# Kernel tuning notes

Measured on AMD Instinct MI355X. Metric: run time of the kernel, lower is better.

Reference implementation:

```python
import jax, jax.numpy as jnp
import numpy as np

KH, KW, STRIDE, PAD, DIL = 3, 3, 1, 1, 1


def setup_inputs() -> dict:
    key = jax.random.key(0)
    ks = jax.random.split(key, 4)
    B, C, H, W, O = 4, 256, 64, 64, 256
    K = KH * KW
    x = jax.random.normal(ks[0], (B, C, H, W), jnp.float32)
    # offset/mask conv params (original inits to zero; use small random so offsets are non-trivial)
    w_om = jax.random.normal(ks[1], (3 * K, C, KH, KW), jnp.float32) * 0.01
    b_om = jnp.zeros((3 * K,), jnp.float32)
    # main weight: kaiming_uniform_(a=1) -> gain = sqrt(2/(1+1^2)) = 1, bound = sqrt(3)/sqrt(fan_in)
    fan_in = C * K
    bound = float(np.sqrt(3.0) / np.sqrt(fan_in))
    weight = jax.random.uniform(ks[2], (O, C, KH, KW), jnp.float32, -bound, bound)
    bias = jnp.zeros((O,), jnp.float32)
    return {"x": x, "w_om": w_om, "b_om": b_om, "weight": weight, "bias": bias}


def _deform_conv2d(x, offset, mask, weight, bias):
    # torchvision.ops.deform_conv2d semantics, deformable_groups=1, stride=1, pad=1, dil=1
    B, C, H, W = x.shape
    K = KH * KW
    # torchvision offset layout: per-tap interleaved (y, x) pairs along channel dim
    off_y = offset[:, 0::2]  # [B, K, H, W]
    off_x = offset[:, 1::2]  # [B, K, H, W]
    ky = (jnp.repeat(jnp.arange(KH), KW) * DIL).astype(x.dtype)  # [K]
    kx = (jnp.tile(jnp.arange(KW), KH) * DIL).astype(x.dtype)    # [K]
    base_y = (jnp.arange(H) * STRIDE - PAD).astype(x.dtype)
    base_x = (jnp.arange(W) * STRIDE - PAD).astype(x.dtype)
    py = base_y[None, None, :, None] + ky[None, :, None, None] + off_y  # [B,K,H,W]
    px = base_x[None, None, None, :] + kx[None, :, None, None] + off_x  # [B,K,H,W]
    y0 = jnp.floor(py)
    x0 = jnp.floor(px)
    ly = py - y0
    lx = px - x0
    y0i = y0.astype(jnp.int32)
    x0i = x0.astype(jnp.int32)
    x_flat = x.reshape(B, C, H * W)

    def gather(yy, xx):
        # zero-padded gather of one bilinear corner -> [B, C, K, H, W]
        valid = ((yy >= 0) & (yy < H) & (xx >= 0) & (xx < W)).astype(x.dtype)
        idx = (jnp.clip(yy, 0, H - 1) * W + jnp.clip(xx, 0, W - 1)).reshape(B, -1)
        g = jax.vmap(lambda xf, i: jnp.take(xf, i, axis=1))(x_flat, idx)
        return g.reshape(B, C, K, H, W) * valid.reshape(B, 1, K, H, W)

    w00 = ((1 - ly) * (1 - lx))[:, None]
    w01 = ((1 - ly) * lx)[:, None]
    w10 = (ly * (1 - lx))[:, None]
    w11 = (ly * lx)[:, None]
    val = (gather(y0i, x0i) * w00 + gather(y0i, x0i + 1) * w01
           + gather(y0i + 1, x0i) * w10 + gather(y0i + 1, x0i + 1) * w11)
    cols = val * mask[:, None]  # modulated columns [B,C,K,H,W]
    out = jnp.einsum('bckhw,ock->bohw', cols, weight.reshape(weight.shape[0], C, K))
    return out + bias[None, :, None, None]


def reference(x, w_om, b_om, weight, bias):
    om = jax.lax.conv_general_dilated(
        x, w_om, (STRIDE, STRIDE), ((PAD, PAD), (PAD, PAD)),
        rhs_dilation=(DIL, DIL), dimension_numbers=('NCHW', 'OIHW', 'NCHW'),
    ) + b_om[None, :, None, None]
    K = KH * KW
    o1, o2, m = om[:, :K], om[:, K:2 * K], om[:, 2 * K:]
    offset = jnp.concatenate([o1, o2], axis=1)  # [B, 2K, H, W]
    mask = jax.nn.sigmoid(m)                    # [B, K, H, W]
    return _deform_conv2d(x, offset, mask, weight, bias)
```

## Files before the change

### kernel.cpp

```cpp
#include <hip/hip_runtime.h>
#include <stdint.h>

#define B_ 4
#define C_ 256
#define H_ 64
#define W_ 64
#define O_ 256
#define K_ 9
#define CK 2304
#define HW 4096
#define NTOT 16384

typedef __bf16 bf16x8 __attribute__((ext_vector_type(8)));
typedef __bf16 bf16x4 __attribute__((ext_vector_type(4)));
typedef float f32x4 __attribute__((ext_vector_type(4)));
typedef float f32x2 __attribute__((ext_vector_type(2)));
typedef f32x2 __attribute__((aligned(4))) f32x2u;

__device__ __forceinline__ uint16_t f2bf(float f) {
  uint32_t u = __builtin_bit_cast(uint32_t, f);
  return (uint16_t)((u + 0x7FFFu + ((u >> 16) & 1u)) >> 16);
}

__device__ __forceinline__ uint32_t pk_bf16(float a, float b) {
  uint16_t lo = __builtin_bit_cast(uint16_t, (__bf16)a);
  uint16_t hi = __builtin_bit_cast(uint16_t, (__bf16)b);
  return (uint32_t)lo | ((uint32_t)hi << 16);
}

__global__ void k0_wconv(const float* __restrict__ weight, uint16_t* __restrict__ wb) {
  int idx = blockIdx.x * 256 + threadIdx.x;
  if (idx >= O_ * CK) return;
  int o = idx / CK;
  int rem = idx - o * CK;
  int k = rem >> 8;
  int c = rem & 255;
  wb[idx] = f2bf(weight[(o * C_ + c) * K_ + k]);
}

__global__ void k0b_womb(const float* __restrict__ w_om, uint16_t* __restrict__ womb) {
  int idx = blockIdx.x * 256 + threadIdx.x;
  if (idx >= 32 * CK) return;
  int j = idx / CK;
  int ck = idx - j * CK;
  int k = ck >> 8, c = ck & 255;
  womb[idx] = (j < 27) ? f2bf(w_om[(j * 256 + c) * 9 + k]) : (uint16_t)0;
}

__global__ void k2a_xT(const float* __restrict__ x, uint16_t* __restrict__ xT) {
  int bx = blockIdx.x;
  int ct = bx & 3;
  int hwt = (bx >> 2) & 63;
  int b = bx >> 8;
  int t = threadIdx.x;
  int l = t & 63;
  int cq = t >> 6;

  __shared__ __align__(16) uint16_t tile[64 * 72];

  const float* xb = x + ((b * 256 + ct * 64) * HW) + hwt * 64;
#pragma unroll
  for (int i = 0; i < 16; ++i) {
    int c = cq * 16 + i;
    tile[l * 72 + c] = f2bf(xb[c * HW + l]);
  }
  __syncthreads();

  int hw = t >> 2;
  int c8 = (t & 3) * 8;
  uint16_t* dst = xT + ((size_t)b << 20) + (size_t)(hwt * 64 + hw) * 256 + ct * 64;
  *(uint4*)&dst[c8] = *(const uint4*)&tile[hw * 72 + c8];
  *(uint4*)&dst[c8 + 32] = *(const uint4*)&tile[hw * 72 + c8 + 32];
}

__global__ void k1_mfma(const uint16_t* __restrict__ womb, const uint16_t* __restrict__ xT,
                        float* __restrict__ ompart) {
  int bx = blockIdx.x;
  int ks = bx >> 8;
  int nt = bx & 255;
  int t = threadIdx.x;
  int lane = t & 63;
  int wid = t >> 6;
  int lr = lane & 15, q = lane >> 4;
  int n = nt * 64 + wid * 16 + lr;
  int b = n >> 12;
  int hw = n & 4095;
  int y = hw >> 6, xx = hw & 63;
  const uint16_t* xb = xT + ((size_t)b << 20);
  const uint16_t* zrow = womb + 31 * CK;

  f32x4 acc0 = {0.f, 0.f, 0.f, 0.f};
  f32x4 acc1 = {0.f, 0.f, 0.f, 0.f};

  for (int kk = 0; kk < 3; ++kk) {
    int k = ks * 3 + kk;
    int dy = k / 3, dx = k - dy * 3;
    int ny = y + dy - 1, nx = xx + dx - 1;
    bool valid = ((unsigned)ny < 64u) && ((unsigned)nx < 64u);
    int row = (min(max(ny, 0), 63) << 6) + min(max(nx, 0), 63);
    const uint16_t* bp = valid ? (xb + row * 256 + q * 8) : (zrow + q * 8);
    const uint16_t* ap = womb + lr * CK + k * 256 + q * 8;
#pragma unroll
    for (int kt = 0; kt < 8; ++kt) {
      int c0 = kt * 32;
      bf16x8 bF = *(const bf16x8*)&bp[c0];
      bf16x8 aF0 = *(const bf16x8*)&ap[c0];
      bf16x8 aF1 = *(const bf16x8*)&ap[16 * CK + c0];
      acc0 = __builtin_amdgcn_mfma_f32_16x16x32_bf16(aF0, bF, acc0, 0, 0, 0);
      acc1 = __builtin_amdgcn_mfma_f32_16x16x32_bf16(aF1, bF, acc1, 0, 0, 0);
    }
  }

  float* op = ompart + ks * (32 * NTOT);
#pragma unroll
  for (int r = 0; r < 4; ++r) {
    op[(q * 4 + r) * NTOT + n] = acc0[r];
    op[(16 + q * 4 + r) * NTOT + n] = acc1[r];
  }
}

__global__ void k1b_ppm(const float* __restrict__ ompart, const float* __restrict__ b_om,
                        float* __restrict__ pypxmk) {
  int tid = blockIdx.x * 256 + threadIdx.x;
  int k = tid >> 14;
  int n = tid & 16383;
  int b = n >> 12;
  int hw = n & 4095;
  int h = hw >> 6, w = hw & 63;
  const float* p0 = ompart;
  const float* p1 = ompart + 32 * NTOT;
  const float* p2 = ompart + 64 * NTOT;
  int iy = (2 * k) * NTOT + n;
  int ix = (2 * k + 1) * NTOT + n;
  int im = (18 + k) * NTOT + n;
  float oy = p0[iy] + p1[iy] + p2[iy] + b_om[2 * k];
  float ox = p0[ix] + p1[ix] + p2[ix] + b_om[2 * k + 1];
  float m = p0[im] + p1[im] + p2[im] + b_om[18 + k];
  int off = (b * 9 + k) * HW + hw;
  pypxmk[off] = (float)(h - 1 + k / 3) + oy;
  pypxmk[147456 + off] = (float)(w - 1 + k % 3) + ox;
  pypxmk[294912 + off] = 1.f / (1.f + __expf(-m));
}

__global__ void k1_offconv(const float* __restrict__ x, const float* __restrict__ w_om,
                           const float* __restrict__ b_om, float* __restrict__ pypxmk) {
  int bx = blockIdx.x;
  int jq = bx % 7;
  int h = (bx / 7) % H_;
  int b = bx / (7 * H_);
  int t = threadIdx.x;
  int w = t & 63;
  int cs = __builtin_amdgcn_readfirstlane(t >> 6);

  float acc[4] = {0.f, 0.f, 0.f, 0.f};
  const float* xb = x + (b * C_) * HW;

  for (int ci = 0; ci < 64; ++ci) {
    int c = cs * 64 + ci;
    const float* xr = xb + c * HW;
    float xv[3][3];
#pragma unroll
    for (int r = 0; r < 3; ++r) {
      int y = h - 1 + r;
      bool yv = ((unsigned)y < 64u);
#pragma unroll
      for (int dx = 0; dx < 3; ++dx) {
        int xx = w - 1 + dx;
        bool v = yv && ((unsigned)xx < 64u);
        xv[r][dx] = v ? xr[y * 64 + xx] : 0.f;
      }
    }
    const float* wp = w_om + ((jq * 4) * C_ + c) * 9;
#pragma unroll
    for (int jj = 0; jj < 4; ++jj) {
      int j = jq * 4 + jj;
      int jeff = (j < 27) ? jj : 0;
      const float* wj = wp + jeff * (C_ * 9);
      float a = 0.f;
#pragma unroll
      for (int r = 0; r < 3; ++r)
#pragma unroll
        for (int dx = 0; dx < 3; ++dx)
          a = fmaf(xv[r][dx], wj[r * 3 + dx], a);
      acc[jj] += a;
    }
  }

  __shared__ float red[4][4][64];
#pragma unroll
  for (int jj = 0; jj < 4; ++jj) red[cs][jj][w] = acc[jj];
  __syncthreads();

  int jj = t >> 6;
  int j = jq * 4 + jj;
  if (j < 27) {
    float s = red[0][jj][w] + red[1][jj][w] + red[2][jj][w] + red[3][jj][w] + b_om[j];
    float* pyA = pypxmk;
    float* pxA = pypxmk + 147456;
    float* mkA = pypxmk + 294912;
    if (j < 18) {
      int k = j >> 1;
      int off = (b * 9 + k) * HW + h * 64 + w;
      if ((j & 1) == 0)
        pyA[off] = (float)(h - 1 + k / 3) + s;
      else
        pxA[off] = (float)(w - 1 + k % 3) + s;
    } else {
      int k = j - 18;
      mkA[(b * 9 + k) * HW + h * 64 + w] = 1.f / (1.f + __expf(-s));
    }
  }
}

__global__ void k2_cols(const uint16_t* __restrict__ xT, const float* __restrict__ pypxmk,
                        uint16_t* __restrict__ cols) {
  int bx = blockIdx.x;
  int g = __builtin_amdgcn_readfirstlane(threadIdx.x >> 6);
  int lane = threadIdx.x & 63;

  const float* pyA = pypxmk;
  const float* pxA = pypxmk + 147456;
  const float* mkA = pypxmk + 294912;

  for (int it = 0; it < 18; ++it) {
    int p = it * 4 + g;
    int pn = p / 9;
    int k = p - pn * 9;
    int n = (bx << 3) + pn;
    int b = n >> 12;
    int hw = n & 4095;
    int poff = (b * 9 + k) * HW + hw;
    float py = pyA[poff];
    float px = pxA[poff];
    float mk = mkA[poff];

    float fy0 = floorf(py), fx0 = floorf(px);
    float ly = py - fy0, lx = px - fx0;
    int y0 = (int)fy0, x0 = (int)fx0;
    bool vy0 = ((unsigned)y0 < 64u), vy1 = ((unsigned)(y0 + 1) < 64u);
    bool vx0 = ((unsigned)x0 < 64u), vx1 = ((unsigned)(x0 + 1) < 64u);
    float w00 = (vy0 && vx0) ? (1.f - ly) * (1.f - lx) * mk : 0.f;
    float w01 = (vy0 && vx1) ? (1.f - ly) * lx * mk : 0.f;
    float w10 = (vy1 && vx0) ? ly * (1.f - lx) * mk : 0.f;
    float w11 = (vy1 && vx1) ? ly * lx * mk : 0.f;
    bool sel0 = (x0 >= 63);
    bool sel1 = (x0 >= 0);
    float wa0 = (sel0 ? 0.f : w00) + (sel1 ? 0.f : w01);
    float wb0 = (sel0 ? w00 : 0.f) + (sel1 ? w01 : 0.f);
    float wa1 = (sel0 ? 0.f : w10) + (sel1 ? 0.f : w11);
    float wb1 = (sel0 ? w10 : 0.f) + (sel1 ? w11 : 0.f);
    int bx0 = min(max(x0, 0), 62);
    int a0 = min(max(y0, 0), 63) * 64 + bx0;
    int a1 = min(max(y0 + 1, 0), 63) * 64 + bx0;

    const uint16_t* xb = xT + ((size_t)b << 20);
    bf16x4 r00 = *(const bf16x4*)&xb[a0 * 256 + lane * 4];
    bf16x4 r01 = *(const bf16x4*)&xb[a0 * 256 + 256 + lane * 4];
    bf16x4 r10 = *(const bf16x4*)&xb[a1 * 256 + lane * 4];
    bf16x4 r11 = *(const bf16x4*)&xb[a1 * 256 + 256 + lane * 4];

    float v[4];
#pragma unroll
    for (int i = 0; i < 4; ++i)
      v[i] = wa0 * (float)r00[i] + wb0 * (float)r01[i] +
             wa1 * (float)r10[i] + wb1 * (float)r11[i];

    uint2 pk;
    pk.x = pk_bf16(v[0], v[1]);
    pk.y = pk_bf16(v[2], v[3]);
    *(uint2*)&cols[(size_t)n * CK + k * 256 + lane * 4] = pk;
  }
}

__global__ void k2_fb(const float* __restrict__ x, const float* __restrict__ pypxmk,
                      uint16_t* __restrict__ cols) {
  int bx = blockIdx.x;
  int cg = bx & 15;
  int h = (bx >> 4) & 63;
  int b = bx >> 10;
  int t = threadIdx.x;
  int w = t & 63;
  int g = t >> 6;

  const float* pyA = pypxmk;
  const float* pxA = pypxmk + 147456;
  const float* mkA = pypxmk + 294912;

  __shared__ uint16_t tile[64 * 146];
  const float* xb = x + b * C_ * HW;
  int cbase = cg * 16 + g * 4;

#pragma unroll
  for (int k = 0; k < 9; ++k) {
    int poff = (b * 9 + k) * HW + h * 64 + w;
    float py = pyA[poff];
    float px = pxA[poff];
    float mk = mkA[poff];
    float fy0 = floorf(py), fx0 = floorf(px);
    float ly = py - fy0, lx = px - fx0;
    int y0 = (int)fy0, x0 = (int)fx0;
    bool vy0 = ((unsigned)y0 < 64u), vy1 = ((unsigned)(y0 + 1) < 64u);
    bool vx0 = ((unsigned)x0 < 64u), vx1 = ((unsigned)(x0 + 1) < 64u);
    float w00 = (vy0 && vx0) ? (1.f - ly) * (1.f - lx) * mk : 0.f;
    float w01 = (vy0 && vx1) ? (1.f - ly) * lx * mk : 0.f;
    float w10 = (vy1 && vx0) ? ly * (1.f - lx) * mk : 0.f;
    float w11 = (vy1 && vx1) ? ly * lx * mk : 0.f;
    bool sel0 = (x0 >= 63);
    bool sel1 = (x0 >= 0);
    float wa0 = (sel0 ? 0.f : w00) + (sel1 ? 0.f : w01);
    float wb0 = (sel0 ? w00 : 0.f) + (sel1 ? w01 : 0.f);
    float wa1 = (sel0 ? 0.f : w10) + (sel1 ? 0.f : w11);
    float wb1 = (sel0 ? w10 : 0.f) + (sel1 ? w11 : 0.f);
    int bx0 = min(max(x0, 0), 62);
    int a0 = min(max(y0, 0), 63) * 64 + bx0;
    int a1 = min(max(y0 + 1, 0), 63) * 64 + bx0;

#pragma unroll
    for (int cp = 0; cp < 2; ++cp) {
      const float* xcA = xb + (cbase + cp * 2) * HW;
      const float* xcB = xcA + HW;
      f32x2 A0 = *(const f32x2u*)&xcA[a0];
      f32x2 A1 = *(const f32x2u*)&xcA[a1];
      f32x2 B0 = *(const f32x2u*)&xcB[a0];
      f32x2 B1 = *(const f32x2u*)&xcB[a1];
      float rA = wa0 * A0.x + wb0 * A0.y + wa1 * A1.x + wb1 * A1.y;
      float rB = wa0 * B0.x + wb0 * B0.y + wa1 * B1.x + wb1 * B1.y;
      *(uint32_t*)&tile[w * 146 + k * 16 + g * 4 + cp * 2] = pk_bf16(rA, rB);
    }
  }
  __syncthreads();

#pragma unroll
  for (int it = 0; it < 18; ++it) {
    int u = t + it * 256;
    int wu = u / 72;
    int rem = u - wu * 72;
    int k = rem >> 3;
    int cd = rem & 7;
    uint32_t val = *(const uint32_t*)&tile[wu * 146 + rem * 2];
    int n = b * HW + h * 64 + wu;
    int dst = n * CK + k * 256 + cg * 16 + cd * 2;
    *(uint32_t*)&cols[dst] = val;
  }
}

__global__ void k3_gemm(const uint16_t* __restrict__ wb, const uint16_t* __restrict__ cols,
                        const float* __restrict__ bias, float* __restrict__ dst,
                        int ktn, int withBias) {
  int bx = blockIdx.x;
  int ks = bx >> 8;
  int bxx = bx & 255;
  int mt = bxx & 1;
  int nt = bxx >> 1;
  int o0 = mt * 128;
  int n0 = nt * 128;
  int t = threadIdx.x;
  int lane = t & 63;
  int wid = t >> 6;
  int wm = wid >> 1, wn = wid & 1;
  int lr = lane & 15, q = lane >> 4;

  __shared__ __align__(16) uint16_t As[128 * 32];
  __shared__ __align__(16) uint16_t Bs[128 * 32];

  f32x4 acc[4][4];
  const f32x4 zero = {0.f, 0.f, 0.f, 0.f};
#pragma unroll
  for (int i = 0; i < 4; ++i)
#pragma unroll
    for (int j = 0; j < 4; ++j) acc[i][j] = zero;

  int r0 = t >> 2;
  int koff = (t & 3) * 8;
  int kb = ks * ktn * 32;
  const uint16_t* gA = wb + (o0 + r0) * CK + kb + koff;
  const uint16_t* gB = cols + (n0 + r0) * CK + kb + koff;

  for (int kt = 0; kt < ktn; ++kt) {
    int k0 = kt * 32;
    __builtin_amdgcn_global_load_lds(
        (const __attribute__((address_space(1))) uint32_t*)(gA + k0),
        (__attribute__((address_space(3))) uint32_t*)&As[t * 8], 16, 0, 0);
    __builtin_amdgcn_global_load_lds(
        (const __attribute__((address_space(1))) uint32_t*)(gA + 64 * CK + k0),
        (__attribute__((address_space(3))) uint32_t*)&As[2048 + t * 8], 16, 0, 0);
    __builtin_amdgcn_global_load_lds(
        (const __attribute__((address_space(1))) uint32_t*)(gB + k0),
        (__attribute__((address_space(3))) uint32_t*)&Bs[t * 8], 16, 0, 0);
    __builtin_amdgcn_global_load_lds(
        (const __attribute__((address_space(1))) uint32_t*)(gB + 64 * CK + k0),
        (__attribute__((address_space(3))) uint32_t*)&Bs[2048 + t * 8], 16, 0, 0);
    __syncthreads();

    bf16x8 aF[4], bF[4];
#pragma unroll
    for (int i = 0; i < 4; ++i)
      aF[i] = *(const bf16x8*)&As[(wm * 64 + i * 16 + lr) * 32 + q * 8];
#pragma unroll
    for (int j = 0; j < 4; ++j)
      bF[j] = *(const bf16x8*)&Bs[(wn * 64 + j * 16 + lr) * 32 + q * 8];
#pragma unroll
    for (int i = 0; i < 4; ++i)
#pragma unroll
      for (int j = 0; j < 4; ++j)
        acc[i][j] = __builtin_amdgcn_mfma_f32_16x16x32_bf16(aF[i], bF[j], acc[i][j], 0, 0, 0);
    __syncthreads();
  }

  float* base = dst + ks * (O_ * NTOT);
  int bb = n0 >> 12;
  int hw0 = n0 & 4095;
#pragma unroll
  for (int i = 0; i < 4; ++i) {
#pragma unroll
    for (int r = 0; r < 4; ++r) {
      int o = o0 + wm * 64 + i * 16 + q * 4 + r;
      float bv = withBias ? bias[o] : 0.f;
      float* orow = base + (bb * O_ + o) * HW + hw0;
#pragma unroll
      for (int j = 0; j < 4; ++j) orow[wn * 64 + j * 16 + lr] = acc[i][j][r] + bv;
    }
  }
}

__global__ void k4_reduce(const float* __restrict__ part, const float* __restrict__ bias,
                          float* __restrict__ out) {
  int i4 = blockIdx.x * 256 + threadIdx.x;
  const f32x4* p0 = (const f32x4*)part;
  const f32x4* p1 = p0 + (O_ * NTOT / 4);
  const f32x4* p2 = p1 + (O_ * NTOT / 4);
  f32x4 a = p0[i4] + p1[i4] + p2[i4];
  int o = (i4 >> 10) & 255;
  ((f32x4*)out)[i4] = a + bias[o];
}

extern "C" void kernel_launch(void* const* d_in, const int* in_sizes, int n_in,
                              void* d_out, int out_size, void* d_ws, size_t ws_size,
                              hipStream_t stream) {
  const float* x = (const float*)d_in[0];
  const float* w_om = (const float*)d_in[1];
  const float* b_om = (const float*)d_in[2];
  const float* weight = (const float*)d_in[3];
  const float* bias = (const float*)d_in[4];
  float* out = (float*)d_out;

  char* ws = (char*)d_ws;
  float* pypxmk = (float*)ws;
  uint16_t* wb = (uint16_t*)(ws + 1769472);
  uint16_t* cols = (uint16_t*)(ws + 2949120);
  uint16_t* xT = (uint16_t*)(ws + 78446592);
  uint16_t* womb = (uint16_t*)(ws + 86835200);
  float* ompart = (float*)(ws + 86982656);
  float* part = (float*)(ws + 93274112);

  bool xtpath = ws_size >= 86835200ull;
  bool mfmak1 = ws_size >= 93274112ull;
  bool splitk = ws_size >= 143605760ull;

  hipLaunchKernelGGL(k0_wconv, dim3(2304), dim3(256), 0, stream, weight, wb);

  if (xtpath) hipLaunchKernelGGL(k2a_xT, dim3(1024), dim3(256), 0, stream, x, xT);

  if (xtpath && mfmak1) {
    hipLaunchKernelGGL(k0b_womb, dim3(288), dim3(256), 0, stream, w_om, womb);
    hipLaunchKernelGGL(k1_mfma, dim3(768), dim3(256), 0, stream, womb, xT, ompart);
    hipLaunchKernelGGL(k1b_ppm, dim3(576), dim3(256), 0, stream, ompart, b_om, pypxmk);
  } else {
    hipLaunchKernelGGL(k1_offconv, dim3(4 * 64 * 7), dim3(256), 0, stream, x, w_om, b_om, pypxmk);
  }

  if (xtpath) {
    hipLaunchKernelGGL(k2_cols, dim3(2048), dim3(256), 0, stream, xT, pypxmk, cols);
  } else {
    hipLaunchKernelGGL(k2_fb, dim3(4 * 64 * 16), dim3(256), 0, stream, x, pypxmk, cols);
  }

  if (splitk) {
    hipLaunchKernelGGL(k3_gemm, dim3(768), dim3(256), 0, stream, wb, cols, bias, part, 24, 0);
    hipLaunchKernelGGL(k4_reduce, dim3(4096), dim3(256), 0, stream, part, bias, out);
  } else {
    hipLaunchKernelGGL(k3_gemm, dim3(256), dim3(256), 0, stream, wb, cols, bias, out, 72, 1);
  }
}
```

Baseline: 180.4 us.

## Fuse prep kernels, fold offset reduction into cols, drop split-K GEMM

Merges the three conversion kernels (weight, offset-weight, x transpose) into one launch. Folds the offset/mask partial-sum reduction and sigmoid into the column-sampling kernel, removing the separate ppm pass and its intermediate buffer. Replaces the split-K GEMM plus reduce with a single full-K GEMM using 128x64 tiles and 512 blocks, which avoids writing and re-reading partial outputs. The trade-off is longer per-block K loops and recomputing the three-way sum once per tap inside the cols kernel.

```diff
diff --git a/kernel.cpp b/kernel.cpp
--- a/kernel.cpp
+++ b/kernel.cpp
@@ -28,49 +28,47 @@
   return (uint32_t)lo | ((uint32_t)hi << 16);
 }
 
-__global__ void k0_wconv(const float* __restrict__ weight, uint16_t* __restrict__ wb) {
-  int idx = blockIdx.x * 256 + threadIdx.x;
-  if (idx >= O_ * CK) return;
-  int o = idx / CK;
-  int rem = idx - o * CK;
-  int k = rem >> 8;
-  int c = rem & 255;
-  wb[idx] = f2bf(weight[(o * C_ + c) * K_ + k]);
-}
-
-__global__ void k0b_womb(const float* __restrict__ w_om, uint16_t* __restrict__ womb) {
-  int idx = blockIdx.x * 256 + threadIdx.x;
-  if (idx >= 32 * CK) return;
-  int j = idx / CK;
-  int ck = idx - j * CK;
-  int k = ck >> 8, c = ck & 255;
-  womb[idx] = (j < 27) ? f2bf(w_om[(j * 256 + c) * 9 + k]) : (uint16_t)0;
-}
-
-__global__ void k2a_xT(const float* __restrict__ x, uint16_t* __restrict__ xT) {
-  int bx = blockIdx.x;
-  int ct = bx & 3;
-  int hwt = (bx >> 2) & 63;
-  int b = bx >> 8;
+__global__ void kA_prep(const float* __restrict__ weight, const float* __restrict__ w_om,
+                        const float* __restrict__ x, uint16_t* __restrict__ wb,
+                        uint16_t* __restrict__ womb, uint16_t* __restrict__ xT) {
+  int bx = blockIdx.x;
   int t = threadIdx.x;
-  int l = t & 63;
-  int cq = t >> 6;
-
-  __shared__ __align__(16) uint16_t tile[64 * 72];
-
-  const float* xb = x + ((b * 256 + ct * 64) * HW) + hwt * 64;
-#pragma unroll
-  for (int i = 0; i < 16; ++i) {
-    int c = cq * 16 + i;
-    tile[l * 72 + c] = f2bf(xb[c * HW + l]);
-  }
-  __syncthreads();
-
-  int hw = t >> 2;
-  int c8 = (t & 3) * 8;
-  uint16_t* dst = xT + ((size_t)b << 20) + (size_t)(hwt * 64 + hw) * 256 + ct * 64;
-  *(uint4*)&dst[c8] = *(const uint4*)&tile[hw * 72 + c8];
-  *(uint4*)&dst[c8 + 32] = *(const uint4*)&tile[hw * 72 + c8 + 32];
+  if (bx < 2304) {
+    int idx = bx * 256 + t;
+    int o = idx / CK;
+    int rem = idx - o * CK;
+    int k = rem >> 8, c = rem & 255;
+    wb[idx] = f2bf(weight[(o * C_ + c) * K_ + k]);
+  } else if (bx < 2592) {
+    int idx = (bx - 2304) * 256 + t;
+    int j = idx / CK;
+    int ck = idx - j * CK;
+    int k = ck >> 8, c = ck & 255;
+    womb[idx] = (j < 27) ? f2bf(w_om[(j * 256 + c) * 9 + k]) : (uint16_t)0;
+  } else {
+    int bxl = bx - 2592;
+    int ct = bxl & 3;
+    int hwt = (bxl >> 2) & 63;
+    int b = bxl >> 8;
+    int l = t & 63;
+    int cq = t >> 6;
+
+    __shared__ __align__(16) uint16_t tile[64 * 72];
+
+    const float* xb = x + ((b * 256 + ct * 64) * HW) + hwt * 64;
+#pragma unroll
+    for (int i = 0; i < 16; ++i) {
+      int c = cq * 16 + i;
+      tile[l * 72 + c] = f2bf(xb[c * HW + l]);
+    }
+    __syncthreads();
+
+    int hw = t >> 2;
+    int c8 = (t & 3) * 8;
+    uint16_t* dst = xT + ((size_t)b << 20) + (size_t)(hwt * 64 + hw) * 256 + ct * 64;
+    *(uint4*)&dst[c8] = *(const uint4*)&tile[hw * 72 + c8];
+    *(uint4*)&dst[c8 + 32] = *(const uint4*)&tile[hw * 72 + c8 + 32];
+  }
 }
 
 __global__ void k1_mfma(const uint16_t* __restrict__ womb, const uint16_t* __restrict__ xT,
@@ -119,108 +117,15 @@
   }
 }
 
-__global__ void k1b_ppm(const float* __restrict__ ompart, const float* __restrict__ b_om,
-                        float* __restrict__ pypxmk) {
-  int tid = blockIdx.x * 256 + threadIdx.x;
-  int k = tid >> 14;
-  int n = tid & 16383;
-  int b = n >> 12;
-  int hw = n & 4095;
-  int h = hw >> 6, w = hw & 63;
-  const float* p0 = ompart;
-  const float* p1 = ompart + 32 * NTOT;
-  const float* p2 = ompart + 64 * NTOT;
-  int iy = (2 * k) * NTOT + n;
-  int ix = (2 * k + 1) * NTOT + n;
-  int im = (18 + k) * NTOT + n;
-  float oy = p0[iy] + p1[iy] + p2[iy] + b_om[2 * k];
-  float ox = p0[ix] + p1[ix] + p2[ix] + b_om[2 * k + 1];
-  float m = p0[im] + p1[im] + p2[im] + b_om[18 + k];
-  int off = (b * 9 + k) * HW + hw;
-  pypxmk[off] = (float)(h - 1 + k / 3) + oy;
-  pypxmk[147456 + off] = (float)(w - 1 + k % 3) + ox;
-  pypxmk[294912 + off] = 1.f / (1.f + __expf(-m));
-}
-
-__global__ void k1_offconv(const float* __restrict__ x, const float* __restrict__ w_om,
-                           const float* __restrict__ b_om, float* __restrict__ pypxmk) {
-  int bx = blockIdx.x;
-  int jq = bx % 7;
-  int h = (bx / 7) % H_;
-  int b = bx / (7 * H_);
-  int t = threadIdx.x;
-  int w = t & 63;
-  int cs = __builtin_amdgcn_readfirstlane(t >> 6);
-
-  float acc[4] = {0.f, 0.f, 0.f, 0.f};
-  const float* xb = x + (b * C_) * HW;
-
-  for (int ci = 0; ci < 64; ++ci) {
-    int c = cs * 64 + ci;
-    const float* xr = xb + c * HW;
-    float xv[3][3];
-#pragma unroll
-    for (int r = 0; r < 3; ++r) {
-      int y = h - 1 + r;
-      bool yv = ((unsigned)y < 64u);
-#pragma unroll
-      for (int dx = 0; dx < 3; ++dx) {
-        int xx = w - 1 + dx;
-        bool v = yv && ((unsigned)xx < 64u);
-        xv[r][dx] = v ? xr[y * 64 + xx] : 0.f;
-      }
-    }
-    const float* wp = w_om + ((jq * 4) * C_ + c) * 9;
-#pragma unroll
-    for (int jj = 0; jj < 4; ++jj) {
-      int j = jq * 4 + jj;
-      int jeff = (j < 27) ? jj : 0;
-      const float* wj = wp + jeff * (C_ * 9);
-      float a = 0.f;
-#pragma unroll
-      for (int r = 0; r < 3; ++r)
-#pragma unroll
-        for (int dx = 0; dx < 3; ++dx)
-          a = fmaf(xv[r][dx], wj[r * 3 + dx], a);
-      acc[jj] += a;
-    }
-  }
-
-  __shared__ float red[4][4][64];
-#pragma unroll
-  for (int jj = 0; jj < 4; ++jj) red[cs][jj][w] = acc[jj];
-  __syncthreads();
-
-  int jj = t >> 6;
-  int j = jq * 4 + jj;
-  if (j < 27) {
-    float s = red[0][jj][w] + red[1][jj][w] + red[2][jj][w] + red[3][jj][w] + b_om[j];
-    float* pyA = pypxmk;
-    float* pxA = pypxmk + 147456;
-    float* mkA = pypxmk + 294912;
-    if (j < 18) {
-      int k = j >> 1;
-      int off = (b * 9 + k) * HW + h * 64 + w;
-      if ((j & 1) == 0)
-        pyA[off] = (float)(h - 1 + k / 3) + s;
-      else
-        pxA[off] = (float)(w - 1 + k % 3) + s;
-    } else {
-      int k = j - 18;
-      mkA[(b * 9 + k) * HW + h * 64 + w] = 1.f / (1.f + __expf(-s));
-    }
-  }
-}
-
-__global__ void k2_cols(const uint16_t* __restrict__ xT, const float* __restrict__ pypxmk,
-                        uint16_t* __restrict__ cols) {
+__global__ void k2_cols(const uint16_t* __restrict__ xT, const float* __restrict__ ompart,
+                        const float* __restrict__ b_om, uint16_t* __restrict__ cols) {
   int bx = blockIdx.x;
   int g = __builtin_amdgcn_readfirstlane(threadIdx.x >> 6);
   int lane = threadIdx.x & 63;
 
-  const float* pyA = pypxmk;
-  const float* pxA = pypxmk + 147456;
-  const float* mkA = pypxmk + 294912;
+  const float* op0 = ompart;
+  const float* op1 = ompart + 32 * NTOT;
+  const float* op2 = ompart + 64 * NTOT;
 
   for (int it = 0; it < 18; ++it) {
     int p = it * 4 + g;
@@ -229,10 +134,18 @@
     int n = (bx << 3) + pn;
     int b = n >> 12;
     int hw = n & 4095;
-    int poff = (b * 9 + k) * HW + hw;
-    float py = pyA[poff];
-    float px = pxA[poff];
-    float mk = mkA[poff];
+    int h = hw >> 6, w = hw & 63;
+
+    int iy = (2 * k) * NTOT + n;
+    int ix = iy + NTOT;
+    int im = (18 + k) * NTOT + n;
+    float oy = op0[iy] + op1[iy] + op2[iy] + b_om[2 * k];
+    float ox = op0[ix] + op1[ix] + op2[ix] + b_om[2 * k + 1];
+    float m = op0[im] + op1[im] + op2[im] + b_om[18 + k];
+    int dy = k / 3, dx = k - dy * 3;
+    float py = (float)(h - 1 + dy) + oy;
+    float px = (float)(w - 1 + dx) + ox;
+    float mk = 1.f / (1.f + __expf(-m));
 
     float fy0 = floorf(py), fx0 = floorf(px);
     float ly = py - fy0, lx = px - fx0;
@@ -269,6 +182,157 @@
     pk.x = pk_bf16(v[0], v[1]);
     pk.y = pk_bf16(v[2], v[3]);
     *(uint2*)&cols[(size_t)n * CK + k * 256 + lane * 4] = pk;
+  }
+}
+
+__global__ void k3_gemm(const uint16_t* __restrict__ wb, const uint16_t* __restrict__ cols,
+                        const float* __restrict__ bias, float* __restrict__ out) {
+  int bx = blockIdx.x;
+  int mt = bx & 1;
+  int nt = bx >> 1;
+  int o0 = mt * 128;
+  int n0 = nt * 64;
+  int t = threadIdx.x;
+  int lane = t & 63;
+  int wid = t >> 6;
+  int wm = wid >> 1, wn = wid & 1;
+  int lr = lane & 15, q = lane >> 4;
+
+  __shared__ __align__(16) uint16_t As[128 * 32];
+  __shared__ __align__(16) uint16_t Bs[64 * 32];
+
+  f32x4 acc[4][2];
+  const f32x4 zero = {0.f, 0.f, 0.f, 0.f};
+#pragma unroll
+  for (int i = 0; i < 4; ++i)
+#pragma unroll
+    for (int j = 0; j < 2; ++j) acc[i][j] = zero;
+
+  int r0 = t >> 2;
+  int koff = (t & 3) * 8;
+  const uint16_t* gA = wb + (o0 + r0) * CK + koff;
+  const uint16_t* gB = cols + (n0 + r0) * CK + koff;
+
+  for (int kt = 0; kt < 72; ++kt) {
+    int k0 = kt * 32;
+    __builtin_amdgcn_global_load_lds(
+        (const __attribute__((address_space(1))) uint32_t*)(gA + k0),
+        (__attribute__((address_space(3))) uint32_t*)&As[t * 8], 16, 0, 0);
+    __builtin_amdgcn_global_load_lds(
+        (const __attribute__((address_space(1))) uint32_t*)(gA + 64 * CK + k0),
+        (__attribute__((address_space(3))) uint32_t*)&As[2048 + t * 8], 16, 0, 0);
+    __builtin_amdgcn_global_load_lds(
+        (const __attribute__((address_space(1))) uint32_t*)(gB + k0),
+        (__attribute__((address_space(3))) uint32_t*)&Bs[t * 8], 16, 0, 0);
+    __syncthreads();
+
+    bf16x8 aF[4], bF[2];
+#pragma unroll
+    for (int i = 0; i < 4; ++i)
+      aF[i] = *(const bf16x8*)&As[(wm * 64 + i * 16 + lr) * 32 + q * 8];
+#pragma unroll
+    for (int j = 0; j < 2; ++j)
+      bF[j] = *(const bf16x8*)&Bs[(wn * 32 + j * 16 + lr) * 32 + q * 8];
+#pragma unroll
+    for (int i = 0; i < 4; ++i)
+#pragma unroll
+      for (int j = 0; j < 2; ++j)
+        acc[i][j] = __builtin_amdgcn_mfma_f32_16x16x32_bf16(aF[i], bF[j], acc[i][j], 0, 0, 0);
+    __syncthreads();
+  }
+
+  int bb = n0 >> 12;
+  int hw0 = n0 & 4095;
+#pragma unroll
+  for (int i = 0; i < 4; ++i) {
+#pragma unroll
+    for (int r = 0; r < 4; ++r) {
+      int o = o0 + wm * 64 + i * 16 + q * 4 + r;
+      float bv = bias[o];
+      float* orow = out + (bb * O_ + o) * HW + hw0;
+#pragma unroll
+      for (int j = 0; j < 2; ++j) orow[wn * 32 + j * 16 + lr] = acc[i][j][r] + bv;
+    }
+  }
+}
+
+__global__ void k0_wconv(const float* __restrict__ weight, uint16_t* __restrict__ wb) {
+  int idx = blockIdx.x * 256 + threadIdx.x;
+  if (idx >= O_ * CK) return;
+  int o = idx / CK;
+  int rem = idx - o * CK;
+  int k = rem >> 8;
+  int c = rem & 255;
+  wb[idx] = f2bf(weight[(o * C_ + c) * K_ + k]);
+}
+
+__global__ void k1_offconv(const float* __restrict__ x, const float* __restrict__ w_om,
+                           const float* __restrict__ b_om, float* __restrict__ pypxmk) {
+  int bx = blockIdx.x;
+  int jq = bx % 7;
+  int h = (bx / 7) % H_;
+  int b = bx / (7 * H_);
+  int t = threadIdx.x;
+  int w = t & 63;
+  int cs = __builtin_amdgcn_readfirstlane(t >> 6);
+
+  float acc[4] = {0.f, 0.f, 0.f, 0.f};
+  const float* xb = x + (b * C_) * HW;
+
+  for (int ci = 0; ci < 64; ++ci) {
+    int c = cs * 64 + ci;
+    const float* xr = xb + c * HW;
+    float xv[3][3];
+#pragma unroll
+    for (int r = 0; r < 3; ++r) {
+      int y = h - 1 + r;
+      bool yv = ((unsigned)y < 64u);
+#pragma unroll
+      for (int dx = 0; dx < 3; ++dx) {
+        int xx = w - 1 + dx;
+        bool v = yv && ((unsigned)xx < 64u);
+        xv[r][dx] = v ? xr[y * 64 + xx] : 0.f;
+      }
+    }
+    const float* wp = w_om + ((jq * 4) * C_ + c) * 9;
+#pragma unroll
+    for (int jj = 0; jj < 4; ++jj) {
+      int j = jq * 4 + jj;
+      int jeff = (j < 27) ? jj : 0;
+      const float* wj = wp + jeff * (C_ * 9);
+      float a = 0.f;
+#pragma unroll
+      for (int r = 0; r < 3; ++r)
+#pragma unroll
+        for (int dx = 0; dx < 3; ++dx)
+          a = fmaf(xv[r][dx], wj[r * 3 + dx], a);
+      acc[jj] += a;
+    }
+  }
+
+  __shared__ float red[4][4][64];
+#pragma unroll
+  for (int jj = 0; jj < 4; ++jj) red[cs][jj][w] = acc[jj];
+  __syncthreads();
+
+  int jj = t >> 6;
+  int j = jq * 4 + jj;
+  if (j < 27) {
+    float s = red[0][jj][w] + red[1][jj][w] + red[2][jj][w] + red[3][jj][w] + b_om[j];
+    float* pyA = pypxmk;
+    float* pxA = pypxmk + 147456;
+    float* mkA = pypxmk + 294912;
+    if (j < 18) {
+      int k = j >> 1;
+      int off = (b * 9 + k) * HW + h * 64 + w;
+      if ((j & 1) == 0)
+        pyA[off] = (float)(h - 1 + k / 3) + s;
+      else
+        pxA[off] = (float)(w - 1 + k % 3) + s;
+    } else {
+      int k = j - 18;
+      mkA[(b * 9 + k) * HW + h * 64 + w] = 1.f / (1.f + __expf(-s));
+    }
   }
 }
 
@@ -344,14 +408,11 @@
   }
 }
 
-__global__ void k3_gemm(const uint16_t* __restrict__ wb, const uint16_t* __restrict__ cols,
-                        const float* __restrict__ bias, float* __restrict__ dst,
-                        int ktn, int withBias) {
-  int bx = blockIdx.x;
-  int ks = bx >> 8;
-  int bxx = bx & 255;
-  int mt = bxx & 1;
-  int nt = bxx >> 1;
+__global__ void k3_flex(const uint16_t* __restrict__ wb, const uint16_t* __restrict__ cols,
+                        const float* __restrict__ bias, float* __restrict__ out) {
+  int bx = blockIdx.x;
+  int mt = bx & 1;
+  int nt = bx >> 1;
   int o0 = mt * 128;
   int n0 = nt * 128;
   int t = threadIdx.x;
@@ -372,11 +433,10 @@
 
   int r0 = t >> 2;
   int koff = (t & 3) * 8;
-  int kb = ks * ktn * 32;
-  const uint16_t* gA = wb + (o0 + r0) * CK + kb + koff;
-  const uint16_t* gB = cols + (n0 + r0) * CK + kb + koff;
-
-  for (int kt = 0; kt < ktn; ++kt) {
+  const uint16_t* gA = wb + (o0 + r0) * CK + koff;
+  const uint16_t* gB = cols + (n0 + r0) * CK + koff;
+
+  for (int kt = 0; kt < 72; ++kt) {
     int k0 = kt * 32;
     __builtin_amdgcn_global_load_lds(
         (const __attribute__((address_space(1))) uint32_t*)(gA + k0),
@@ -407,7 +467,6 @@
     __syncthreads();
   }
 
-  float* base = dst + ks * (O_ * NTOT);
   int bb = n0 >> 12;
   int hw0 = n0 & 4095;
 #pragma unroll
@@ -415,23 +474,12 @@
 #pragma unroll
     for (int r = 0; r < 4; ++r) {
       int o = o0 + wm * 64 + i * 16 + q * 4 + r;
-      float bv = withBias ? bias[o] : 0.f;
-      float* orow = base + (bb * O_ + o) * HW + hw0;
+      float bv = bias[o];
+      float* orow = out + (bb * O_ + o) * HW + hw0;
 #pragma unroll
       for (int j = 0; j < 4; ++j) orow[wn * 64 + j * 16 + lr] = acc[i][j][r] + bv;
     }
   }
-}
-
-__global__ void k4_reduce(const float* __restrict__ part, const float* __restrict__ bias,
-                          float* __restrict__ out) {
-  int i4 = blockIdx.x * 256 + threadIdx.x;
-  const f32x4* p0 = (const f32x4*)part;
-  const f32x4* p1 = p0 + (O_ * NTOT / 4);
-  const f32x4* p2 = p1 + (O_ * NTOT / 4);
-  f32x4 a = p0[i4] + p1[i4] + p2[i4];
-  int o = (i4 >> 10) & 255;
-  ((f32x4*)out)[i4] = a + bias[o];
 }
 
 extern "C" void kernel_launch(void* const* d_in, const int* in_sizes, int n_in,
@@ -445,40 +493,23 @@
   float* out = (float*)d_out;
 
   char* ws = (char*)d_ws;
-  float* pypxmk = (float*)ws;
-  uint16_t* wb = (uint16_t*)(ws + 1769472);
-  uint16_t* cols = (uint16_t*)(ws + 2949120);
-  uint16_t* xT = (uint16_t*)(ws + 78446592);
-  uint16_t* womb = (uint16_t*)(ws + 86835200);
-  float* ompart = (float*)(ws + 86982656);
-  float* part = (float*)(ws + 93274112);
-
-  bool xtpath = ws_size >= 86835200ull;
-  bool mfmak1 = ws_size >= 93274112ull;
-  bool splitk = ws_size >= 143605760ull;
-
-  hipLaunchKernelGGL(k0_wconv, dim3(2304), dim3(256), 0, stream, weight, wb);
-
-  if (xtpath) hipLaunchKernelGGL(k2a_xT, dim3(1024), dim3(256), 0, stream, x, xT);
-
-  if (xtpath && mfmak1) {
-    hipLaunchKernelGGL(k0b_womb, dim3(288), dim3(256), 0, stream, w_om, womb);
+  uint16_t* wb = (uint16_t*)ws;
+  uint16_t* womb = (uint16_t*)(ws + 1179648);
+  uint16_t* xT = (uint16_t*)(ws + 1327104);
+  float* ompart = (float*)(ws + 9715712);
+  uint16_t* cols = (uint16_t*)(ws + 16007168);
+
+  if (ws_size >= 91504640ull) {
+    hipLaunchKernelGGL(kA_prep, dim3(3616), dim3(256), 0, stream, weight, w_om, x, wb, womb, xT);
     hipLaunchKernelGGL(k1_mfma, dim3(768), dim3(256), 0, stream, womb, xT, ompart);
-    hipLaunchKernelGGL(k1b_ppm, dim3(576), dim3(256), 0, stream, ompart, b_om, pypxmk);
+    hipLaunchKernelGGL(k2_cols, dim3(2048), dim3(256), 0, stream, xT, ompart, b_om, cols);
+    hipLaunchKernelGGL(k3_gemm, dim3(512), dim3(256), 0, stream, wb, cols, bias, out);
   } else {
+    float* pypxmk = (float*)(ws + 1179648);
+    uint16_t* colsf = (uint16_t*)(ws + 2949120);
+    hipLaunchKernelGGL(k0_wconv, dim3(2304), dim3(256), 0, stream, weight, wb);
     hipLaunchKernelGGL(k1_offconv, dim3(4 * 64 * 7), dim3(256), 0, stream, x, w_om, b_om, pypxmk);
-  }
-
-  if (xtpath) {
-    hipLaunchKernelGGL(k2_cols, dim3(2048), dim3(256), 0, stream, xT, pypxmk, cols);
-  } else {
-    hipLaunchKernelGGL(k2_fb, dim3(4 * 64 * 16), dim3(256), 0, stream, x, pypxmk, cols);
-  }
-
-  if (splitk) {
-    hipLaunchKernelGGL(k3_gemm, dim3(768), dim3(256), 0, stream, wb, cols, bias, part, 24, 0);
-    hipLaunchKernelGGL(k4_reduce, dim3(4096), dim3(256), 0, stream, part, bias, out);
-  } else {
-    hipLaunchKernelGGL(k3_gemm, dim3(256), dim3(256), 0, stream, wb, cols, bias, out, 72, 1);
-  }
-}
+    hipLaunchKernelGGL(k2_fb, dim3(4 * 64 * 16), dim3(256), 0, stream, x, pypxmk, colsf);
+    hipLaunchKernelGGL(k3_flex, dim3(256), dim3(256), 0, stream, wb, colsf, bias, out);
+  }
+}
```

Result: slower. 229.7 us (+27.3%).
